# Optimization experiments

Hardware: AMD Instinct MI355X
Metric: run time of the kernel (lower is better)

Reference implementation:

```python
import jax, jax.numpy as jnp
import numpy as np

INV_SQRT_2 = 0.5 ** 0.5


def setup_inputs() -> dict:
    key = jax.random.key(0)
    k1, k2, k3, k4, k5 = jax.random.split(key, 5)
    B, N, E, D_IN, D_OUT = 2, 50000, 800000, 64, 64
    x = jax.random.normal(k1, (B, N, D_IN), dtype=jnp.float32)
    src = jax.random.randint(k2, (E,), 0, N, dtype=jnp.int64)
    dst = jax.random.randint(k3, (E,), 0, N, dtype=jnp.int64)
    # nn.Linear weights: (dim_out, dim_in), bias=False
    W_src = jax.random.normal(k4, (D_OUT, D_IN), dtype=jnp.float32) / np.sqrt(D_IN)
    W_dst = jax.random.normal(k5, (D_OUT, D_IN), dtype=jnp.float32) / np.sqrt(D_IN)
    return {"x": x, "src": src, "dst": dst, "W_src": W_src, "W_dst": W_dst}


def reference(x, src, dst, W_src, W_dst):
    # Equivalent math to linear(x[:, src]) + linear(x[:, dst]):
    # transform each node once, then gather per edge (avoids redundant GEMM work).
    hs = jnp.einsum('bnd,ed->bne', x, W_src)  # (B, N, D_out)
    hd = jnp.einsum('bnd,ed->bne', x, W_dst)  # (B, N, D_out)
    return (hs[:, src] + hd[:, dst]) * INV_SQRT_2  # (B, E, D_out)
```

## Files before the change

kernel.cpp:

```cpp
#include <hip/hip_runtime.h>

#define INV_SQRT2 0.70710678118654752440f

typedef __attribute__((ext_vector_type(8))) short bf16x8;
typedef __attribute__((ext_vector_type(4))) float f32x4;
typedef __attribute__((ext_vector_type(8))) unsigned short u16x8;

__device__ __forceinline__ unsigned short f32_to_bf16_rne(float f) {
    unsigned int u = __builtin_bit_cast(unsigned int, f);
    u += 0x7FFFu + ((u >> 16) & 1u);
    return (unsigned short)(u >> 16);
}
__device__ __forceinline__ float bf16_to_f32(unsigned short h) {
    return __builtin_bit_cast(float, ((unsigned int)h) << 16);
}

__global__ __launch_bounds__(256) void convert_w_k(
    const float* __restrict__ Wsrc,
    const float* __restrict__ Wdst,
    unsigned short* __restrict__ Wb)
{
    int t = blockIdx.x * 256 + threadIdx.x;
    if (t >= 1024) return;
    int base = t * 8;

    const float* sp = (base < 4096) ? (Wsrc + base) : (Wdst + (base - 4096));
    unsigned short* dp = Wb + base;

    float4 a = ((const float4*)sp)[0];
    float4 b = ((const float4*)sp)[1];
    uint4 o;
    o.x = (unsigned)f32_to_bf16_rne(a.x) | ((unsigned)f32_to_bf16_rne(a.y) << 16);
    o.y = (unsigned)f32_to_bf16_rne(a.z) | ((unsigned)f32_to_bf16_rne(a.w) << 16);
    o.z = (unsigned)f32_to_bf16_rne(b.x) | ((unsigned)f32_to_bf16_rne(b.y) << 16);
    o.w = (unsigned)f32_to_bf16_rne(b.z) | ((unsigned)f32_to_bf16_rne(b.w) << 16);
    *((uint4*)dp) = o;
}

__global__ __launch_bounds__(256) void transform_mfma_k(
    const float* __restrict__ x,
    const unsigned short* __restrict__ Wb,
    unsigned short* __restrict__ hb,
    int rows)
{
    int wave = (blockIdx.x * 256 + threadIdx.x) >> 6;
    int lane = threadIdx.x & 63;
    int row_tiles = (rows + 15) >> 4;
    if (wave >= row_tiles) return;

    int m    = lane & 15;
    int quad = lane >> 4;

    int arow_i = wave * 16 + m;
    if (arow_i >= rows) arow_i = rows - 1;
    const float4* arow = (const float4*)(x + (size_t)arow_i * 64);
    float4 f0 = arow[quad * 2];
    float4 f1 = arow[quad * 2 + 1];
    float4 f2 = arow[8 + quad * 2];
    float4 f3 = arow[8 + quad * 2 + 1];

    bf16x8 a0, a1;
    a0[0] = (short)f32_to_bf16_rne(f0.x);
    a0[1] = (short)f32_to_bf16_rne(f0.y);
    a0[2] = (short)f32_to_bf16_rne(f0.z);
    a0[3] = (short)f32_to_bf16_rne(f0.w);
    a0[4] = (short)f32_to_bf16_rne(f1.x);
    a0[5] = (short)f32_to_bf16_rne(f1.y);
    a0[6] = (short)f32_to_bf16_rne(f1.z);
    a0[7] = (short)f32_to_bf16_rne(f1.w);
    a1[0] = (short)f32_to_bf16_rne(f2.x);
    a1[1] = (short)f32_to_bf16_rne(f2.y);
    a1[2] = (short)f32_to_bf16_rne(f2.z);
    a1[3] = (short)f32_to_bf16_rne(f2.w);
    a1[4] = (short)f32_to_bf16_rne(f3.x);
    a1[5] = (short)f32_to_bf16_rne(f3.y);
    a1[6] = (short)f32_to_bf16_rne(f3.z);
    a1[7] = (short)f32_to_bf16_rne(f3.w);

    f32x4 acc[8];
#pragma unroll
    for (int ct = 0; ct < 8; ++ct) {
        int n = ct * 16 + m;
        const bf16x8* brow = (const bf16x8*)(Wb + (size_t)n * 64);
        bf16x8 b0 = brow[quad];
        bf16x8 b1 = brow[4 + quad];
        f32x4 c = {0.f, 0.f, 0.f, 0.f};
        c = __builtin_amdgcn_mfma_f32_16x16x32_bf16(a0, b0, c, 0, 0, 0);
        c = __builtin_amdgcn_mfma_f32_16x16x32_bf16(a1, b1, c, 0, 0, 0);
        acc[ct] = c;
    }

#pragma unroll
    for (int ct = 0; ct < 8; ++ct) {
#pragma unroll
        for (int r = 0; r < 4; ++r) {
            int orow = wave * 16 + quad * 4 + r;
            if (orow < rows) {
                hb[(size_t)orow * 128 + ct * 16 + m] =
                    f32_to_bf16_rne(acc[ct][r] * INV_SQRT2);
            }
        }
    }
}

__device__ __forceinline__ void sum_store(const u16x8 a, const u16x8 b,
                                          f32x4* __restrict__ out, size_t o4)
{
    f32x4 lo, hi;
    lo[0] = bf16_to_f32(a[0]) + bf16_to_f32(b[0]);
    lo[1] = bf16_to_f32(a[1]) + bf16_to_f32(b[1]);
    lo[2] = bf16_to_f32(a[2]) + bf16_to_f32(b[2]);
    lo[3] = bf16_to_f32(a[3]) + bf16_to_f32(b[3]);
    hi[0] = bf16_to_f32(a[4]) + bf16_to_f32(b[4]);
    hi[1] = bf16_to_f32(a[5]) + bf16_to_f32(b[5]);
    hi[2] = bf16_to_f32(a[6]) + bf16_to_f32(b[6]);
    hi[3] = bf16_to_f32(a[7]) + bf16_to_f32(b[7]);
    __builtin_nontemporal_store(lo, &out[o4]);
    __builtin_nontemporal_store(hi, &out[o4 + 1]);
}

__global__ __launch_bounds__(256) void gather_k(
    const unsigned short* __restrict__ hb,
    const int* __restrict__ src,
    const int* __restrict__ dst,
    f32x4* __restrict__ out,
    int E, int N)
{
    int t = blockIdx.x * 256 + threadIdx.x;
    if (t >= E * 4) return;
    int p = t >> 3;
    int c = t & 7;
    int e0 = p * 2;

    int2 sp = *(const int2*)(src + e0);
    int2 dp = *(const int2*)(dst + e0);

    const unsigned short* h0 = hb;
    const unsigned short* h1 = hb + (size_t)N * 128;
    const int off = c * 8;

    u16x8 us0a = *(const u16x8*)(h0 + (size_t)sp.x * 128 + off);
    u16x8 ud0a = *(const u16x8*)(h0 + (size_t)dp.x * 128 + 64 + off);
    u16x8 us1a = *(const u16x8*)(h1 + (size_t)sp.x * 128 + off);
    u16x8 ud1a = *(const u16x8*)(h1 + (size_t)dp.x * 128 + 64 + off);
    u16x8 us0b = *(const u16x8*)(h0 + (size_t)sp.y * 128 + off);
    u16x8 ud0b = *(const u16x8*)(h0 + (size_t)dp.y * 128 + 64 + off);
    u16x8 us1b = *(const u16x8*)(h1 + (size_t)sp.y * 128 + off);
    u16x8 ud1b = *(const u16x8*)(h1 + (size_t)dp.y * 128 + 64 + off);

    size_t c2 = (size_t)(c * 2);
    sum_store(us0a, ud0a, out, (size_t)e0 * 16 + c2);
    sum_store(us1a, ud1a, out, ((size_t)E + e0) * 16 + c2);
    sum_store(us0b, ud0b, out, (size_t)(e0 + 1) * 16 + c2);
    sum_store(us1b, ud1b, out, ((size_t)E + e0 + 1) * 16 + c2);
}

__global__ __launch_bounds__(256) void fused_fallback_k(
    const float* __restrict__ x,
    const int* __restrict__ src,
    const int* __restrict__ dst,
    const float* __restrict__ Wsrc,
    const float* __restrict__ Wdst,
    float* __restrict__ out,
    int E, int N)
{
    int t = blockIdx.x * 256 + threadIdx.x;
    if (t >= E * 64) return;
    int o = t & 63;
    int e = t >> 6;
    int b = blockIdx.y;

    const float* xs = x + ((size_t)(b * N + src[e])) * 64;
    const float* xd = x + ((size_t)(b * N + dst[e])) * 64;
    const float* ws = Wsrc + o * 64;
    const float* wd = Wdst + o * 64;
    float acc = 0.0f;
#pragma unroll
    for (int k = 0; k < 64; ++k) {
        acc = fmaf(xs[k], ws[k], acc);
        acc = fmaf(xd[k], wd[k], acc);
    }
    out[((size_t)b * E + e) * 64 + o] = acc * INV_SQRT2;
}

extern "C" void kernel_launch(void* const* d_in, const int* in_sizes, int n_in,
                              void* d_out, int out_size, void* d_ws, size_t ws_size,
                              hipStream_t stream)
{
    const float* x    = (const float*)d_in[0];
    const int*   src  = (const int*)d_in[1];
    const int*   dst  = (const int*)d_in[2];
    const float* Wsrc = (const float*)d_in[3];
    const float* Wdst = (const float*)d_in[4];
    float* out = (float*)d_out;

    const int E = in_sizes[1];
    const long long xsz = in_sizes[0];
    const int B = (int)((long long)out_size / ((long long)E * 64));
    const int N = (int)(xsz / ((long long)B * 64));
    const int rows = B * N;

    const size_t wb_elems = 128 * 64;
    const size_t hb_elems = (size_t)rows * 128;
    const size_t need = (wb_elems + hb_elems) * sizeof(unsigned short);

    if (ws_size >= need && B == 2 && (E & 1) == 0) {
        unsigned short* Wb = (unsigned short*)d_ws;
        unsigned short* hb = Wb + wb_elems;

        convert_w_k<<<4, 256, 0, stream>>>(Wsrc, Wdst, Wb);

        int row_tiles = (rows + 15) >> 4;
        int g1 = (row_tiles + 3) / 4;
        transform_mfma_k<<<g1, 256, 0, stream>>>(x, Wb, hb, rows);

        int g2 = (E * 4 + 255) / 256;
        gather_k<<<g2, 256, 0, stream>>>(hb, src, dst, (f32x4*)out, E, N);
    } else {
        dim3 g((E * 64 + 255) / 256, B);
        fused_fallback_k<<<g, 256, 0, stream>>>(x, src, dst, Wsrc, Wdst, out, E, N);
    }
}
```

Before: 505.9 us.

## Interleave both batches per node row so each gather fetches one 512-byte row

The transformed node table is rearranged so each node's row holds the source projections for both batches followed by the destination projections for both batches (256 bf16 values). The gather kernel now runs twice as many threads, each handling one batch half and doing four loads instead of eight, so the random src/dst lookups for both batches land in one contiguous row. The aim is to improve cache-line and DRAM-page locality of the random gathers and to raise parallelism. In exchange, the transform kernel's stores become more scattered, and the gather threads issue fewer loads each.

After: 496.6 us. No clear change (-1.8%).

```diff
diff --git a/kernel.cpp b/kernel.cpp
--- a/kernel.cpp
+++ b/kernel.cpp
@@ -40,8 +40,8 @@
 __global__ __launch_bounds__(256) void transform_mfma_k(
     const float* __restrict__ x,
     const unsigned short* __restrict__ Wb,
-    unsigned short* __restrict__ hb,
-    int rows)
+    unsigned short* __restrict__ ht,
+    int rows, int N)
 {
     int wave = (blockIdx.x * 256 + threadIdx.x) >> 6;
     int lane = threadIdx.x & 63;
@@ -92,11 +92,16 @@
 
 #pragma unroll
     for (int ct = 0; ct < 8; ++ct) {
+        int col = ct * 16 + m;
+        int seg = col >> 6;
+        int cc  = col & 63;
 #pragma unroll
         for (int r = 0; r < 4; ++r) {
             int orow = wave * 16 + quad * 4 + r;
             if (orow < rows) {
-                hb[(size_t)orow * 128 + ct * 16 + m] =
+                int b = (orow >= N) ? 1 : 0;
+                int n = orow - b * N;
+                ht[(size_t)n * 256 + seg * 128 + b * 64 + cc] =
                     f32_to_bf16_rne(acc[ct][r] * INV_SQRT2);
             }
         }
@@ -120,39 +125,35 @@
 }
 
 __global__ __launch_bounds__(256) void gather_k(
-    const unsigned short* __restrict__ hb,
+    const unsigned short* __restrict__ ht,
     const int* __restrict__ src,
     const int* __restrict__ dst,
     f32x4* __restrict__ out,
     int E, int N)
 {
     int t = blockIdx.x * 256 + threadIdx.x;
-    if (t >= E * 4) return;
-    int p = t >> 3;
-    int c = t & 7;
+    if (t >= E * 8) return;
+    int p = t >> 4;
+    int c = t & 15;
     int e0 = p * 2;
 
     int2 sp = *(const int2*)(src + e0);
     int2 dp = *(const int2*)(dst + e0);
 
-    const unsigned short* h0 = hb;
-    const unsigned short* h1 = hb + (size_t)N * 128;
-    const int off = c * 8;
-
-    u16x8 us0a = *(const u16x8*)(h0 + (size_t)sp.x * 128 + off);
-    u16x8 ud0a = *(const u16x8*)(h0 + (size_t)dp.x * 128 + 64 + off);
-    u16x8 us1a = *(const u16x8*)(h1 + (size_t)sp.x * 128 + off);
-    u16x8 ud1a = *(const u16x8*)(h1 + (size_t)dp.x * 128 + 64 + off);
-    u16x8 us0b = *(const u16x8*)(h0 + (size_t)sp.y * 128 + off);
-    u16x8 ud0b = *(const u16x8*)(h0 + (size_t)dp.y * 128 + 64 + off);
-    u16x8 us1b = *(const u16x8*)(h1 + (size_t)sp.y * 128 + off);
-    u16x8 ud1b = *(const u16x8*)(h1 + (size_t)dp.y * 128 + 64 + off);
-
-    size_t c2 = (size_t)(c * 2);
-    sum_store(us0a, ud0a, out, (size_t)e0 * 16 + c2);
-    sum_store(us1a, ud1a, out, ((size_t)E + e0) * 16 + c2);
-    sum_store(us0b, ud0b, out, (size_t)(e0 + 1) * 16 + c2);
-    sum_store(us1b, ud1b, out, ((size_t)E + e0 + 1) * 16 + c2);
+    int b    = c >> 3;
+    int cc   = (c & 7) * 8;
+    int soff = b * 64 + cc;
+    int doff = 128 + b * 64 + cc;
+
+    u16x8 sa = *(const u16x8*)(ht + (size_t)sp.x * 256 + soff);
+    u16x8 da = *(const u16x8*)(ht + (size_t)dp.x * 256 + doff);
+    u16x8 sb = *(const u16x8*)(ht + (size_t)sp.y * 256 + soff);
+    u16x8 db = *(const u16x8*)(ht + (size_t)dp.y * 256 + doff);
+
+    size_t oa = (((size_t)b * E + e0) * 64 + cc) >> 2;
+    sum_store(sa, da, out, oa);
+    size_t ob = (((size_t)b * E + e0 + 1) * 64 + cc) >> 2;
+    sum_store(sb, db, out, ob);
 }
 
 __global__ __launch_bounds__(256) void fused_fallback_k(
@@ -201,21 +202,21 @@
     const int rows = B * N;
 
     const size_t wb_elems = 128 * 64;
-    const size_t hb_elems = (size_t)rows * 128;
-    const size_t need = (wb_elems + hb_elems) * sizeof(unsigned short);
+    const size_t ht_elems = (size_t)N * 256;
+    const size_t need = (wb_elems + ht_elems) * sizeof(unsigned short);
 
     if (ws_size >= need && B == 2 && (E & 1) == 0) {
         unsigned short* Wb = (unsigned short*)d_ws;
-        unsigned short* hb = Wb + wb_elems;
+        unsigned short* ht = Wb + wb_elems;
 
         convert_w_k<<<4, 256, 0, stream>>>(Wsrc, Wdst, Wb);
 
         int row_tiles = (rows + 15) >> 4;
         int g1 = (row_tiles + 3) / 4;
-        transform_mfma_k<<<g1, 256, 0, stream>>>(x, Wb, hb, rows);
-
-        int g2 = (E * 4 + 255) / 256;
-        gather_k<<<g2, 256, 0, stream>>>(hb, src, dst, (f32x4*)out, E, N);
+        transform_mfma_k<<<g1, 256, 0, stream>>>(x, Wb, ht, rows, N);
+
+        int g2 = (E * 8 + 255) / 256;
+        gather_k<<<g2, 256, 0, stream>>>(ht, src, dst, (f32x4*)out, E, N);
     } else {
         dim3 g((E * 64 + 255) / 256, B);
         fused_fallback_k<<<g, 256, 0, stream>>>(x, src, dst, Wsrc, Wdst, out, E, N);
```
